# Optimization experiments

Hardware: AMD Instinct MI355X
Metric: run time of the kernel (lower is better)

The kernel has to match this reference:

```python
import jax, jax.numpy as jnp
import numpy as np

DIM = 1024

def setup_inputs() -> dict:
    key = jax.random.key(0)
    k1, k2, k3, k4 = jax.random.split(key, 4)
    x = jax.random.normal(k1, (4, 4096, DIM), dtype=jnp.float32)
    A = jax.random.normal(k2, (DIM, DIM), dtype=jnp.float32) * 0.01
    B_w = jax.random.normal(k3, (DIM, DIM), dtype=jnp.float32) * (1.0 / np.sqrt(DIM))
    C_w = jax.random.normal(k4, (DIM, DIM), dtype=jnp.float32) * (1.0 / np.sqrt(DIM))
    D = jnp.ones((DIM,), dtype=jnp.float32)
    return {"x": x, "A": A, "B_w": B_w, "C_w": C_w, "D": D}

def reference(x, A, B_w, C_w, D):
    # x: [B, L, Dm]; recurrence: h_t = tanh(h_{t-1} @ A.T + x_t @ B_w.T)
    #                 y_t = h_t @ C_w.T + D * x_t
    Bsz, L, Dm = x.shape
    # Precompute the input projection for all steps at once (one big GEMM).
    bx = jnp.einsum('bld,ed->ble', x, B_w)  # [B, L, Dm]

    def step(h, inputs):
        bx_t, x_t = inputs
        h = jnp.tanh(h @ A.T + bx_t)
        y = h @ C_w.T + D * x_t
        return h, y

    h0 = jnp.zeros((Bsz, Dm), dtype=x.dtype)
    # scan over time axis: move L to leading dim
    _, ys = jax.lax.scan(step, h0, (jnp.swapaxes(bx, 0, 1), jnp.swapaxes(x, 0, 1)))
    return jnp.swapaxes(ys, 0, 1)  # [B, L, Dm]
```

## Files before the change

kernel.cpp:

```cpp
#include <hip/hip_runtime.h>
#include <math.h>

#define DM   1024
#define BSZ  4
#define LSEQ 4096
#define GPB  32
#define RPW  32
#define TPB  256
#define SP   132
#define HSW  1056
#define RS   1056

typedef unsigned long long u64;

__global__ __launch_bounds__(TPB) void bx_gemm_kernel(
    const float* __restrict__ X, const float* __restrict__ Bw,
    float* __restrict__ out)
{
    __shared__ float xs[16][68];
    __shared__ float bs[16][68];
    const int bm = blockIdx.x, bn = blockIdx.y;
    const int t  = threadIdx.x;
    const int tx = t & 15, ty = t >> 4;
    const int ml = t >> 2;
    const int kq = (t & 3) * 4;
    const float* xg = X  + (size_t)(bm * 64 + ml) * DM + kq;
    const float* bg = Bw + (size_t)(bn * 64 + ml) * DM + kq;
    float acc[4][4] = {};
    for (int k0 = 0; k0 < DM; k0 += 16) {
        float4 xv = *(const float4*)(xg + k0);
        float4 bv = *(const float4*)(bg + k0);
        __syncthreads();
        xs[kq+0][ml] = xv.x; xs[kq+1][ml] = xv.y; xs[kq+2][ml] = xv.z; xs[kq+3][ml] = xv.w;
        bs[kq+0][ml] = bv.x; bs[kq+1][ml] = bv.y; bs[kq+2][ml] = bv.z; bs[kq+3][ml] = bv.w;
        __syncthreads();
        #pragma unroll
        for (int kk = 0; kk < 16; ++kk) {
            float a[4], c[4];
            #pragma unroll
            for (int i = 0; i < 4; ++i) a[i] = xs[kk][ty*4+i];
            #pragma unroll
            for (int j = 0; j < 4; ++j) c[j] = bs[kk][tx*4+j];
            #pragma unroll
            for (int i = 0; i < 4; ++i)
                #pragma unroll
                for (int j = 0; j < 4; ++j)
                    acc[i][j] += a[i] * c[j];
        }
    }
    #pragma unroll
    for (int i = 0; i < 4; ++i) {
        float4 v = make_float4(acc[i][0], acc[i][1], acc[i][2], acc[i][3]);
        *(float4*)(out + (size_t)(bm*64 + ty*4 + i)*DM + bn*64 + tx*4) = v;
    }
}

__global__ __launch_bounds__(TPB, 1) void scan_kernel(
    const float* __restrict__ A, const float* __restrict__ Cw,
    const float* __restrict__ Dv, const float* __restrict__ X,
    float* __restrict__ Y, u64* hbuf)
{
    extern __shared__ float lds[];
    float* cs = lds;
    float* hs = lds + RPW * RS;
    const int b   = blockIdx.x >> 5;
    const int gw  = blockIdx.x & 31;
    const int r0  = gw * RPW;
    const int t   = threadIdx.x;
    const int row = t >> 3;
    const int seg = t & 7;
    const bool lead = (seg == 0);

    float ra[128];
    {
        const float* Ap = A + (size_t)(r0 + row) * DM + seg * 128;
        #pragma unroll
        for (int u = 0; u < 32; ++u) {
            float4 v = *(const float4*)(Ap + u*4);
            ra[u*4+0]=v.x; ra[u*4+1]=v.y; ra[u*4+2]=v.z; ra[u*4+3]=v.w;
        }
    }
    for (int i = 0; i < 32; ++i) {
        int idx = i * TPB + t;
        int rr  = idx >> 8;
        int c   = (idx & 255) * 4;
        float4 v = *(const float4*)(Cw + (size_t)(r0 + rr) * DM + c);
        *(float4*)(cs + rr * RS + (c >> 7) * SP + (c & 127)) = v;
    }
    const float dv = Dv[r0 + row];
    __syncthreads();

    for (int k = 0; k <= LSEQ; ++k) {
        float bxv = 0.f;
        if (lead && k < LSEQ)
            bxv = Y[(size_t)b*LSEQ*DM + (size_t)k*DM + r0 + row];

        u64* src = hbuf + (size_t)(k & 1) * BSZ * DM + (size_t)b * DM;
        u64 v0 = __hip_atomic_load(src + t,       __ATOMIC_RELAXED, __HIP_MEMORY_SCOPE_AGENT);
        u64 v1 = __hip_atomic_load(src + t + 256, __ATOMIC_RELAXED, __HIP_MEMORY_SCOPE_AGENT);
        u64 v2 = __hip_atomic_load(src + t + 512, __ATOMIC_RELAXED, __HIP_MEMORY_SCOPE_AGENT);
        u64 v3 = __hip_atomic_load(src + t + 768, __ATOMIC_RELAXED, __HIP_MEMORY_SCOPE_AGENT);
        const unsigned tag = (unsigned)k;
        int spins = 0;
        while ((((unsigned)(v0 >> 32)) != tag || ((unsigned)(v1 >> 32)) != tag ||
                ((unsigned)(v2 >> 32)) != tag || ((unsigned)(v3 >> 32)) != tag)
               && ++spins < (1 << 20)) {
            if ((unsigned)(v0 >> 32) != tag)
                v0 = __hip_atomic_load(src + t,       __ATOMIC_RELAXED, __HIP_MEMORY_SCOPE_AGENT);
            if ((unsigned)(v1 >> 32) != tag)
                v1 = __hip_atomic_load(src + t + 256, __ATOMIC_RELAXED, __HIP_MEMORY_SCOPE_AGENT);
            if ((unsigned)(v2 >> 32) != tag)
                v2 = __hip_atomic_load(src + t + 512, __ATOMIC_RELAXED, __HIP_MEMORY_SCOPE_AGENT);
            if ((unsigned)(v3 >> 32) != tag)
                v3 = __hip_atomic_load(src + t + 768, __ATOMIC_RELAXED, __HIP_MEMORY_SCOPE_AGENT);
        }
        {
            int c0 = t, c1 = t + 256, c2 = t + 512, c3 = t + 768;
            hs[(c0 >> 7) * SP + (c0 & 127)] = __uint_as_float((unsigned)v0);
            hs[(c1 >> 7) * SP + (c1 & 127)] = __uint_as_float((unsigned)v1);
            hs[(c2 >> 7) * SP + (c2 & 127)] = __uint_as_float((unsigned)v2);
            hs[(c3 >> 7) * SP + (c3 & 127)] = __uint_as_float((unsigned)v3);
        }
        __syncthreads();

        float accA = 0.f;
        {
            const float4* h4p = (const float4*)(hs + seg * SP);
            #pragma unroll
            for (int u = 0; u < 32; ++u) {
                float4 h4 = h4p[u];
                accA += ra[u*4+0]*h4.x + ra[u*4+1]*h4.y + ra[u*4+2]*h4.z + ra[u*4+3]*h4.w;
            }
        }
        accA += __shfl_xor(accA, 1);
        accA += __shfl_xor(accA, 2);
        accA += __shfl_xor(accA, 4);
        if (lead && k < LSEQ) {
            float hv = tanhf(accA + bxv);
            u64 pk = ((u64)(unsigned)(k + 1) << 32) | (u64)__float_as_uint(hv);
            __hip_atomic_store(hbuf + (size_t)((k+1) & 1) * BSZ * DM + (size_t)b * DM + r0 + row,
                               pk, __ATOMIC_RELAXED, __HIP_MEMORY_SCOPE_AGENT);
        }

        if (k > 0) {
            float accC = 0.f;
            const float4* c4p = (const float4*)(cs + row * RS + seg * SP);
            const float4* h4p = (const float4*)(hs + seg * SP);
            #pragma unroll
            for (int u = 0; u < 32; ++u) {
                float4 c4 = c4p[u];
                float4 h4 = h4p[u];
                accC += c4.x*h4.x + c4.y*h4.y + c4.z*h4.z + c4.w*h4.w;
            }
            accC += __shfl_xor(accC, 1);
            accC += __shfl_xor(accC, 2);
            accC += __shfl_xor(accC, 4);
            if (lead) {
                const size_t yoff = (size_t)b*LSEQ*DM + (size_t)(k-1)*DM + r0 + row;
                Y[yoff] = accC + dv * X[yoff];
            }
        }
        __syncthreads();
    }
}

extern "C" void kernel_launch(void* const* d_in, const int* in_sizes, int n_in,
                              void* d_out, int out_size, void* d_ws, size_t ws_size,
                              hipStream_t stream)
{
    const float* X  = (const float*)d_in[0];
    const float* A  = (const float*)d_in[1];
    const float* Bw = (const float*)d_in[2];
    const float* Cw = (const float*)d_in[3];
    const float* Dv = (const float*)d_in[4];
    float* Y   = (float*)d_out;
    u64* hbuf  = (u64*)d_ws;

    hipMemsetAsync(d_ws, 0, (size_t)2 * BSZ * DM * sizeof(u64), stream);

    dim3 g1((BSZ * LSEQ) / 64, DM / 64);
    bx_gemm_kernel<<<g1, TPB, 0, stream>>>(X, Bw, Y);
    const size_t lds_bytes = (size_t)(RPW * RS + HSW) * sizeof(float);
    scan_kernel<<<BSZ * GPB, TPB, lds_bytes, stream>>>(A, Cw, Dv, X, Y, hbuf);
}
```

Before: 11.51 ms.

## Halve scan workgroups to 64 rows each and read C_w from global memory

The scan kernel now runs 16 workgroups per batch with 512 threads and 64 rows each, instead of 32 workgroups with 256 threads. This halves the number of workgroups that spin on and synchronise through the global h buffer. The C_w slice is no longer staged in LDS; each thread streams its 128-element C_w row segment from global or cache every step. This cuts LDS use so two workgroups can fit per CU, at the cost of re-reading C_w from cache at every time step. Launch bounds change to (512, 2), which squeezes the per-thread register budget while 128 A coefficients stay in registers and may spill.

```diff
diff --git a/kernel.cpp b/kernel.cpp
--- a/kernel.cpp
+++ b/kernel.cpp
@@ -4,16 +4,15 @@
 #define DM   1024
 #define BSZ  4
 #define LSEQ 4096
-#define GPB  32
-#define RPW  32
-#define TPB  256
+#define GPB  16
+#define RPW  64
+#define TPB  512
 #define SP   132
 #define HSW  1056
-#define RS   1056
 
 typedef unsigned long long u64;
 
-__global__ __launch_bounds__(TPB) void bx_gemm_kernel(
+__global__ __launch_bounds__(256) void bx_gemm_kernel(
     const float* __restrict__ X, const float* __restrict__ Bw,
     float* __restrict__ out)
 {
@@ -55,16 +54,14 @@
     }
 }
 
-__global__ __launch_bounds__(TPB, 1) void scan_kernel(
+__global__ __launch_bounds__(TPB, 2) void scan_kernel(
     const float* __restrict__ A, const float* __restrict__ Cw,
     const float* __restrict__ Dv, const float* __restrict__ X,
     float* __restrict__ Y, u64* hbuf)
 {
-    extern __shared__ float lds[];
-    float* cs = lds;
-    float* hs = lds + RPW * RS;
-    const int b   = blockIdx.x >> 5;
-    const int gw  = blockIdx.x & 31;
+    __shared__ float hs[HSW];
+    const int b   = blockIdx.x >> 4;
+    const int gw  = blockIdx.x & 15;
     const int r0  = gw * RPW;
     const int t   = threadIdx.x;
     const int row = t >> 3;
@@ -80,15 +77,8 @@
             ra[u*4+0]=v.x; ra[u*4+1]=v.y; ra[u*4+2]=v.z; ra[u*4+3]=v.w;
         }
     }
-    for (int i = 0; i < 32; ++i) {
-        int idx = i * TPB + t;
-        int rr  = idx >> 8;
-        int c   = (idx & 255) * 4;
-        float4 v = *(const float4*)(Cw + (size_t)(r0 + rr) * DM + c);
-        *(float4*)(cs + rr * RS + (c >> 7) * SP + (c & 127)) = v;
-    }
-    const float dv = Dv[r0 + row];
-    __syncthreads();
+    const float* Cp = Cw + (size_t)(r0 + row) * DM + seg * 128;
+    const float dv  = Dv[r0 + row];
 
     for (int k = 0; k <= LSEQ; ++k) {
         float bxv = 0.f;
@@ -97,29 +87,20 @@
 
         u64* src = hbuf + (size_t)(k & 1) * BSZ * DM + (size_t)b * DM;
         u64 v0 = __hip_atomic_load(src + t,       __ATOMIC_RELAXED, __HIP_MEMORY_SCOPE_AGENT);
-        u64 v1 = __hip_atomic_load(src + t + 256, __ATOMIC_RELAXED, __HIP_MEMORY_SCOPE_AGENT);
-        u64 v2 = __hip_atomic_load(src + t + 512, __ATOMIC_RELAXED, __HIP_MEMORY_SCOPE_AGENT);
-        u64 v3 = __hip_atomic_load(src + t + 768, __ATOMIC_RELAXED, __HIP_MEMORY_SCOPE_AGENT);
+        u64 v1 = __hip_atomic_load(src + t + 512, __ATOMIC_RELAXED, __HIP_MEMORY_SCOPE_AGENT);
         const unsigned tag = (unsigned)k;
         int spins = 0;
-        while ((((unsigned)(v0 >> 32)) != tag || ((unsigned)(v1 >> 32)) != tag ||
-                ((unsigned)(v2 >> 32)) != tag || ((unsigned)(v3 >> 32)) != tag)
+        while ((((unsigned)(v0 >> 32)) != tag || ((unsigned)(v1 >> 32)) != tag)
                && ++spins < (1 << 20)) {
             if ((unsigned)(v0 >> 32) != tag)
                 v0 = __hip_atomic_load(src + t,       __ATOMIC_RELAXED, __HIP_MEMORY_SCOPE_AGENT);
             if ((unsigned)(v1 >> 32) != tag)
-                v1 = __hip_atomic_load(src + t + 256, __ATOMIC_RELAXED, __HIP_MEMORY_SCOPE_AGENT);
-            if ((unsigned)(v2 >> 32) != tag)
-                v2 = __hip_atomic_load(src + t + 512, __ATOMIC_RELAXED, __HIP_MEMORY_SCOPE_AGENT);
-            if ((unsigned)(v3 >> 32) != tag)
-                v3 = __hip_atomic_load(src + t + 768, __ATOMIC_RELAXED, __HIP_MEMORY_SCOPE_AGENT);
+                v1 = __hip_atomic_load(src + t + 512, __ATOMIC_RELAXED, __HIP_MEMORY_SCOPE_AGENT);
         }
         {
-            int c0 = t, c1 = t + 256, c2 = t + 512, c3 = t + 768;
+            int c0 = t, c1 = t + 512;
             hs[(c0 >> 7) * SP + (c0 & 127)] = __uint_as_float((unsigned)v0);
             hs[(c1 >> 7) * SP + (c1 & 127)] = __uint_as_float((unsigned)v1);
-            hs[(c2 >> 7) * SP + (c2 & 127)] = __uint_as_float((unsigned)v2);
-            hs[(c3 >> 7) * SP + (c3 & 127)] = __uint_as_float((unsigned)v3);
         }
         __syncthreads();
 
@@ -144,11 +125,10 @@
 
         if (k > 0) {
             float accC = 0.f;
-            const float4* c4p = (const float4*)(cs + row * RS + seg * SP);
             const float4* h4p = (const float4*)(hs + seg * SP);
             #pragma unroll
             for (int u = 0; u < 32; ++u) {
-                float4 c4 = c4p[u];
+                float4 c4 = *(const float4*)(Cp + u*4);
                 float4 h4 = h4p[u];
                 accC += c4.x*h4.x + c4.y*h4.y + c4.z*h4.z + c4.w*h4.w;
             }
@@ -179,7 +159,6 @@
     hipMemsetAsync(d_ws, 0, (size_t)2 * BSZ * DM * sizeof(u64), stream);
 
     dim3 g1((BSZ * LSEQ) / 64, DM / 64);
-    bx_gemm_kernel<<<g1, TPB, 0, stream>>>(X, Bw, Y);
-    const size_t lds_bytes = (size_t)(RPW * RS + HSW) * sizeof(float);
-    scan_kernel<<<BSZ * GPB, TPB, lds_bytes, stream>>>(A, Cw, Dv, X, Y, hbuf);
+    bx_gemm_kernel<<<g1, 256, 0, stream>>>(X, Bw, Y);
+    scan_kernel<<<BSZ * GPB, TPB, 0, stream>>>(A, Cw, Dv, X, Y, hbuf);
 }
```

Measured after the change: 37.61 ms. 3.27x slower.
